# Kernel tuning notes

Hardware: AMD Instinct MI355X
Metric: run time of the kernel (lower is better)

The kernel has to match this reference:

```python
import jax, jax.numpy as jnp
import numpy as np

T, A, E, N, W, HID, FD = 4096, 1024, 512, 32768, 10, 150, 20
GI = 2 * A + E  # 2560
BINS = jnp.array([1, 2, 3, 4, 8, 16, 32, 64], dtype=jnp.int32)


def _mlp(x, W1, b1, W2, b2, W3, b3):
    # Score module: Linear->ReLU->Linear->ReLU->Linear->1 (dropout is a no-op in eval)
    h = jax.nn.relu(x @ W1 + b1)
    h = jax.nn.relu(h @ W2 + b2)
    return h @ W3 + b3


def setup_inputs() -> dict:
    key = jax.random.key(0)
    ks = jax.random.split(key, 20)
    s = 0.02
    inp = {
        "states": jax.random.normal(ks[0], (T, A), jnp.float32),
        "embeds": jax.random.normal(ks[1], (T, E), jnp.float32),
        "span_starts": jax.random.randint(ks[2], (N,), 0, T - W, jnp.int32),
        "span_widths": jax.random.randint(ks[3], (N,), 1, W + 1, jnp.int32),
        # attention Score params (input A)
        "Wa1": jax.random.normal(ks[4], (A, HID)) * s, "ba1": jnp.zeros((HID,)),
        "Wa2": jax.random.normal(ks[5], (HID, HID)) * s, "ba2": jnp.zeros((HID,)),
        "Wa3": jax.random.normal(ks[6], (HID, 1)) * s, "ba3": jnp.zeros((1,)),
        # width Feature embedding table: len(bins)+1 = 9 rows
        "width_emb": jax.random.normal(ks[7], (9, FD)) * s,
        # mention Score params (input GI + FD)
        "Ws1": jax.random.normal(ks[8], (GI + FD, HID)) * s, "bs1": jnp.zeros((HID,)),
        "Ws2": jax.random.normal(ks[9], (HID, HID)) * s, "bs2": jnp.zeros((HID,)),
        "Ws3": jax.random.normal(ks[10], (HID, 1)) * s, "bs3": jnp.zeros((1,)),
    }
    return inp


def reference(states, embeds, span_starts, span_widths,
              Wa1, ba1, Wa2, ba2, Wa3, ba3, width_emb,
              Ws1, bs1, Ws2, bs2, Ws3, bs3):
    # per-token attention logits  [T]
    attns = _mlp(states, Wa1, ba1, Wa2, ba2, Wa3, ba3).squeeze(-1)
    offs = jnp.arange(W)                                   # [W]
    pos = span_starts[:, None] + offs[None, :]             # [N, W]
    mask = offs[None, :] < span_widths[:, None]            # ragged span mask
    pos_c = jnp.clip(pos, 0, T - 1)
    logit = jnp.where(mask, attns[pos_c], -jnp.inf)        # [N, W]
    w = jax.nn.softmax(logit, axis=1)                      # per-span softmax
    attn_sum = jnp.einsum('nw,nwe->ne', w, embeds[pos_c])  # [N, E]
    ends = span_starts + span_widths - 1
    bin_idx = jnp.sum(span_widths[:, None] >= BINS[None, :], axis=1)
    size = width_emb[bin_idx]                              # [N, FD]
    g = jnp.concatenate([states[span_starts], states[ends], attn_sum, size], axis=1)
    scores = _mlp(g, Ws1, bs1, Ws2, bs2, Ws3, bs3).squeeze(-1)  # [N]
    return scores
```

## Files before the change

### kernel.cpp

```cpp
#include <hip/hip_runtime.h>
#include <math.h>

#define T_TOK 4096
#define A_DIM 1024
#define E_DIM 512
#define N_SPAN 32768
#define W_MAX 10
#define HID 150
#define FD 20

#define PR  160
#define KP2 160

#define WS_ATTNS 0
#define WS_PB    4096
#define WS_WPACK 1314816
#define WS_SB    1627856
#define WS_EB    3725008
#define PB_P0 0
#define PB_P1 655360
#define PB_P2 1310720
#define PB_P3 1966080
#define WP_ST  0
#define WP_V   491520
#define WP_A2  573440
#define WP_S2  599040
#define WP_WE1 624640
#define WP_TOTAL 626080
#define SB_PIECES 524288
#define EB_PIECES 262144
#define PK_ITEMS (WP_TOTAL + SB_PIECES + EB_PIECES)

typedef short  bf16x8 __attribute__((ext_vector_type(8)));
typedef float  f32x4  __attribute__((ext_vector_type(4)));

__device__ __forceinline__ float4 ld4(const float* p) { return *(const float4*)p; }

__device__ __forceinline__ unsigned short f2bf(float f) {
    unsigned u = __float_as_uint(f);
    unsigned r = u + 0x7fffu + ((u >> 16) & 1u);
    return (unsigned short)(r >> 16);
}
__device__ __forceinline__ float bf2f(short s) {
    return __uint_as_float(((unsigned)(unsigned short)s) << 16);
}
__device__ __forceinline__ bf16x8 cvt_frag(const float* p) {
    float4 u = ld4(p), v = ld4(p + 4);
    bf16x8 f;
    f[0] = (short)f2bf(u.x); f[1] = (short)f2bf(u.y);
    f[2] = (short)f2bf(u.z); f[3] = (short)f2bf(u.w);
    f[4] = (short)f2bf(v.x); f[5] = (short)f2bf(v.y);
    f[6] = (short)f2bf(v.z); f[7] = (short)f2bf(v.w);
    return f;
}

typedef const __attribute__((address_space(1))) unsigned int as1_u32;
typedef __attribute__((address_space(3))) unsigned int as3_u32;
__device__ __forceinline__ void dma16(const void* g, void* l) {
    __builtin_amdgcn_global_load_lds((as1_u32*)g, (as3_u32*)l, 16, 0, 0);
}
template<int N> __device__ __forceinline__ void waitv() {
    asm volatile("s_waitcnt vmcnt(%0)" :: "n"(N) : "memory");
}

__global__ __launch_bounds__(256) void prepack_kernel(
    const float* __restrict__ states, const float* __restrict__ embeds,
    const float* __restrict__ Wa1, const float* __restrict__ Ws1,
    const float* __restrict__ Wa2, const float* __restrict__ Ws2,
    const float* __restrict__ width_emb,
    unsigned short* __restrict__ wp, unsigned short* __restrict__ Sb,
    unsigned short* __restrict__ Eb)
{
    int idx = blockIdx.x * 256 + threadIdx.x;
    if (idx >= PK_ITEMS) return;
    if (idx < WP_TOTAL) {
        float v = 0.f;
        if (idx < WP_V) {
            int gidx = idx / 163840, r = idx % 163840;
            int ngrp = r / 81920, r2 = r % 81920;
            int c = r2 / 2560, d = r2 % 2560;
            int n = d >> 5, qsw = (d >> 3) & 3, off = d & 7;
            int q = qsw ^ ((n >> 1) & 3);
            int k = c * 32 + q * 8 + off;
            int gn = ngrp * 80 + n;
            const float* W = (gidx == 0) ? Wa1 : Ws1 + (size_t)(gidx - 1) * 1024 * HID;
            if (gn < HID) v = W[(size_t)k * HID + gn];
        } else if (idx < WP_A2) {
            int r = idx - WP_V;
            int ngrp = r / 40960, r2 = r % 40960;
            int c = r2 / 2560, d = r2 % 2560;
            int n = d >> 5, qsw = (d >> 3) & 3, off = d & 7;
            int q = qsw ^ ((n >> 1) & 3);
            int k = c * 32 + q * 8 + off;
            int gn = ngrp * 80 + n;
            if (gn < HID) v = Ws1[(size_t)(2048 + k) * HID + gn];
        } else if (idx < WP_S2) {
            int e = idx - WP_A2;
            int n = e / KP2, k = e % KP2;
            if (n < HID && k < HID) v = Wa2[(size_t)k * HID + n];
        } else if (idx < WP_WE1) {
            int e = idx - WP_S2;
            int n = e / KP2, k = e % KP2;
            if (n < HID && k < HID) v = Ws2[(size_t)k * HID + n];
        } else {
            int e = idx - WP_WE1;
            int b = e / KP2, n = e % KP2;
            if (n < HID)
                for (int k = 0; k < FD; ++k)
                    v = fmaf(width_emb[b * FD + k], Ws1[(size_t)(2560 + k) * HID + n], v);
        }
        wp[idx] = f2bf(v);
    } else if (idx < WP_TOTAL + SB_PIECES) {
        int p = idx - WP_TOTAL;
        int mb = p >> 11, r = p & 2047;
        int c = r >> 6, d8 = r & 63;
        int m = d8 >> 2, qsw = d8 & 3;
        int q = qsw ^ ((m >> 1) & 3);
        const float* src = states + (size_t)(mb * 16 + m) * A_DIM + c * 32 + q * 8;
        *(bf16x8*)(Sb + (size_t)p * 8) = cvt_frag(src);
    } else {
        int p = idx - WP_TOTAL - SB_PIECES;
        int mb = p >> 10, r = p & 1023;
        int c = r >> 6, d8 = r & 63;
        int m = d8 >> 2, qsw = d8 & 3;
        int q = qsw ^ ((m >> 1) & 3);
        const float* src = embeds + (size_t)(mb * 16 + m) * E_DIM + c * 32 + q * 8;
        *(bf16x8*)(Eb + (size_t)p * 8) = cvt_frag(src);
    }
}

template<int NC>
__device__ __forceinline__ void gemm_dma(
    const unsigned short* __restrict__ srcA, const unsigned short* __restrict__ srcB,
    unsigned short (*__restrict__ bufB)[2560], unsigned short (*__restrict__ bufA)[512],
    int lane, int l15, int quad, f32x4 (&acc)[5])
{
    const int swz = (quad ^ ((l15 >> 1) & 3)) * 8;
    const int bl = l15 * 32 + swz;
#define DMAC(c) { _Pragma("unroll")                                          \
        for (int i = 0; i < 5; ++i)                                          \
            dma16(srcB + (size_t)(c) * 2560 + i * 512 + lane * 8,            \
                  &bufB[(c) & 3][i * 512]);                                  \
        dma16(srcA + (size_t)(c) * 512 + lane * 8, &bufA[(c) & 3][0]); }
    DMAC(0);
    DMAC(1);
    DMAC(2);
#pragma unroll
    for (int c = 0; c < NC; ++c) {
        if (c + 3 < NC) DMAC(c + 3);
        if (c + 3 < NC)      waitv<18>();
        else if (c + 2 < NC) waitv<12>();
        else if (c + 1 < NC) waitv<6>();
        else                 waitv<0>();
        bf16x8 af = *(const bf16x8*)(&bufA[c & 3][0] + bl);
        const unsigned short* bb = &bufB[c & 3][0];
#pragma unroll
        for (int t = 0; t < 5; ++t) {
            bf16x8 bf = *(const bf16x8*)(bb + t * 512 + bl);
            acc[t] = __builtin_amdgcn_mfma_f32_16x16x32_bf16(af, bf, acc[t], 0, 0, 0);
        }
    }
#undef DMAC
}

__global__ __launch_bounds__(64) void token_kernel(
    const unsigned short* __restrict__ Sb, const unsigned short* __restrict__ Eb,
    const unsigned short* __restrict__ wp, unsigned short* __restrict__ Pb)
{
    __shared__ __align__(16) unsigned short bufB[4][2560];
    __shared__ __align__(16) unsigned short bufA[4][512];

    const int lane = threadIdx.x, l15 = lane & 15, quad = lane >> 4;
    const int task = blockIdx.x;

    f32x4 acc[5];
#pragma unroll
    for (int t = 0; t < 5; ++t)
#pragma unroll
        for (int i = 0; i < 4; ++i) acc[t][i] = 0.f;

    int m0, gidx, ngrp;
    if (task < 1536) {
        const int mb = task / 6;
        m0 = mb * 16;
        const int sub = task % 6;
        gidx = sub >> 1;
        ngrp = sub & 1;
        const unsigned short* srcA = Sb + (size_t)mb * 16384;
        const unsigned short* srcB = wp + WP_ST + gidx * 163840 + ngrp * 81920;
        gemm_dma<32>(srcA, srcB, bufB, bufA, lane, l15, quad, acc);
    } else {
        const int e = task - 1536;
        const int mb = e >> 1;
        m0 = mb * 16;
        ngrp = e & 1;
        gidx = 3;
        const unsigned short* srcA = Eb + (size_t)mb * 8192;
        const unsigned short* srcB = wp + WP_V + ngrp * 40960;
        gemm_dma<16>(srcA, srcB, bufB, bufA, lane, l15, quad, acc);
    }

    unsigned short* Pg = Pb + (size_t)gidx * 655360;
#pragma unroll
    for (int t = 0; t < 5; ++t) {
        const int col = ngrp * 80 + t * 16 + l15;
#pragma unroll
        for (int i = 0; i < 4; ++i)
            Pg[(size_t)(m0 + quad * 4 + i) * PR + col] =
                (col < HID) ? f2bf(acc[t][i]) : (unsigned short)0;
    }
}

__global__ __launch_bounds__(64) void attn_tail_kernel(
    const unsigned short* __restrict__ P0, const float* __restrict__ ba1,
    const unsigned short* __restrict__ wp, const float* __restrict__ ba2,
    const float* __restrict__ Wa3, const float* __restrict__ ba3,
    float* __restrict__ attns)
{
    const int t0 = blockIdx.x * 16;
    const int lane = threadIdx.x, l15 = lane & 15, quad = lane >> 4;

    f32x4 acc[10];
#pragma unroll
    for (int nt = 0; nt < 10; ++nt)
#pragma unroll
        for (int i = 0; i < 4; ++i) acc[nt][i] = 0.f;

    const unsigned short* prow = P0 + (size_t)(t0 + l15) * PR;
    const unsigned short* bb = wp + WP_A2 + l15 * KP2 + quad * 8;

#pragma unroll
    for (int c = 0; c < 5; ++c) {
        const int k0 = c * 32;
        const int kk = k0 + quad * 8;
        bf16x8 raw = *(const bf16x8*)(prow + kk);
        bf16x8 af;
#pragma unroll
        for (int j = 0; j < 8; ++j) {
            const float b = (kk + j < HID) ? ba1[kk + j] : 0.f;
            af[j] = (short)f2bf(fmaxf(bf2f(raw[j]) + b, 0.f));
        }
#pragma unroll
        for (int nt = 0; nt < 10; ++nt) {
            bf16x8 bf = *(const bf16x8*)(bb + nt * 16 * KP2 + k0);
            acc[nt] = __builtin_amdgcn_mfma_f32_16x16x32_bf16(af, bf, acc[nt], 0, 0, 0);
        }
    }

    float sc[4] = {0.f, 0.f, 0.f, 0.f};
#pragma unroll
    for (int nt = 0; nt < 10; ++nt) {
        const int col = nt * 16 + l15;
        const float w3 = (col < HID) ? Wa3[col] : 0.f;
        const float b2 = (col < HID) ? ba2[col] : 0.f;
#pragma unroll
        for (int i = 0; i < 4; ++i)
            sc[i] = fmaf(fmaxf(acc[nt][i] + b2, 0.f), w3, sc[i]);
    }
#pragma unroll
    for (int off = 8; off >= 1; off >>= 1)
#pragma unroll
        for (int i = 0; i < 4; ++i) sc[i] += __shfl_down(sc[i], off, 16);
    if (l15 == 0) {
        const float b3 = ba3[0];
#pragma unroll
        for (int i = 0; i < 4; ++i) attns[t0 + quad * 4 + i] = sc[i] + b3;
    }
}

__global__ __launch_bounds__(256) void span_kernel(
    const unsigned short* __restrict__ Pb, const float* __restrict__ attns,
    const unsigned short* __restrict__ wp,
    const int* __restrict__ span_starts, const int* __restrict__ span_widths,
    const float* __restrict__ bs1, const float* __restrict__ bs2,
    const float* __restrict__ Ws3, const float* __restrict__ bs3,
    float* __restrict__ out)
{
    __shared__ unsigned short sHb[32][168];
    __shared__ float s_wgt[32][W_MAX];
    __shared__ int s_st[32], s_wd[32], s_bin[32], s_oid[32], s_wdr[32];
    __shared__ float sPart[4][32];
    __shared__ float sb1[KP2];

    const int tid = threadIdx.x;
    const int n0s = blockIdx.x * 32;

    if (tid < KP2) sb1[tid] = (tid < HID) ? bs1[tid] : 0.f;
    int st = 0, wd = 0;
    if (tid < 32) {
        st = span_starts[n0s + tid];
        wd = span_widths[n0s + tid];
        s_wdr[tid] = wd;
    }
    __syncthreads();
    if (tid < 32) {
        int rank = 0;
#pragma unroll
        for (int j = 0; j < 32; ++j) {
            const int wj = s_wdr[j];
            rank += (wj < wd) || (wj == wd && j < tid);
        }
        s_st[rank] = st; s_wd[rank] = wd; s_oid[rank] = tid;
        s_bin[rank] = (wd >= 1) + (wd >= 2) + (wd >= 3) + (wd >= 4) +
                      (wd >= 8) + (wd >= 16) + (wd >= 32) + (wd >= 64);
        float lg[W_MAX];
        float m = -1e30f;
#pragma unroll
        for (int w = 0; w < W_MAX; ++w)
            if (w < wd) { float a = attns[st + w]; lg[w] = a; m = fmaxf(m, a); }
        float sum = 0.f;
#pragma unroll
        for (int w = 0; w < W_MAX; ++w) {
            float e = (w < wd) ? __expf(lg[w] - m) : 0.f;
            lg[w] = e; sum += e;
        }
        float inv = 1.f / sum;
#pragma unroll
        for (int w = 0; w < W_MAX; ++w) s_wgt[rank][w] = lg[w] * inv;
    }
    __syncthreads();

    {
        const unsigned short* P1b = Pb + PB_P1;
        const unsigned short* P2b = Pb + PB_P2;
        const unsigned short* P3b = Pb + PB_P3;
        const unsigned short* WEb = wp + WP_WE1;
        const int s = tid >> 3, jl = tid & 7;
        const int sst = s_st[s], swd = s_wd[s];
        const size_t rs = (size_t)sst * PR;
        const size_t re = (size_t)(sst + swd - 1) * PR;
        const size_t rb = (size_t)s_bin[s] * PR;
        for (int c = jl; c < 20; c += 8) {
            const int j = c * 8;
            bf16x8 u1 = *(const bf16x8*)(P1b + rs + j);
            bf16x8 u2 = *(const bf16x8*)(P2b + re + j);
            bf16x8 uw = *(const bf16x8*)(WEb + rb + j);
            float acc[8];
#pragma unroll
            for (int i = 0; i < 8; ++i)
                acc[i] = bf2f(u1[i]) + bf2f(u2[i]) + bf2f(uw[i]) + sb1[j + i];
#pragma unroll
            for (int w = 0; w < W_MAX; ++w) {
                if (w < swd) {
                    float wt = s_wgt[s][w];
                    bf16x8 uv = *(const bf16x8*)(P3b + rs + (size_t)w * PR + j);
#pragma unroll
                    for (int i = 0; i < 8; ++i)
                        acc[i] = fmaf(wt, bf2f(uv[i]), acc[i]);
                }
            }
            bf16x8 pk;
#pragma unroll
            for (int i = 0; i < 8; ++i) pk[i] = (short)f2bf(fmaxf(acc[i], 0.f));
            *(bf16x8*)&sHb[s][j] = pk;
        }
    }
    __syncthreads();

    const int wv = tid >> 6, lane = tid & 63, l15 = lane & 15, quad = lane >> 4;
    const int nb = (wv < 2) ? wv * 3 : 6 + (wv - 2) * 2;
    const int cnt = (wv < 2) ? 3 : 2;

    f32x4 a2[2][3];
#pragma unroll
    for (int mt = 0; mt < 2; ++mt)
#pragma unroll
        for (int t = 0; t < 3; ++t)
#pragma unroll
            for (int i = 0; i < 4; ++i) a2[mt][t][i] = 0.f;

#pragma unroll
    for (int c = 0; c < 5; ++c) {
        int k0 = c * 32;
        bf16x8 af0 = *(const bf16x8*)&sHb[l15][k0 + quad * 8];
        bf16x8 af1 = *(const bf16x8*)&sHb[16 + l15][k0 + quad * 8];
#pragma unroll
        for (int t = 0; t < 3; ++t) {
            if (t < cnt) {
                bf16x8 b = *(const bf16x8*)(wp + WP_S2 +
                            (size_t)((nb + t) * 16 + l15) * KP2 + k0 + quad * 8);
                a2[0][t] = __builtin_amdgcn_mfma_f32_16x16x32_bf16(af0, b, a2[0][t], 0, 0, 0);
                a2[1][t] = __builtin_amdgcn_mfma_f32_16x16x32_bf16(af1, b, a2[1][t], 0, 0, 0);
            }
        }
    }

    float sc[2][4];
#pragma unroll
    for (int mt = 0; mt < 2; ++mt)
#pragma unroll
        for (int i = 0; i < 4; ++i) sc[mt][i] = 0.f;
#pragma unroll
    for (int t = 0; t < 3; ++t) {
        if (t < cnt) {
            int col = (nb + t) * 16 + l15;
            float w3 = (col < HID) ? Ws3[col] : 0.f;
            float b2 = (col < HID) ? bs2[col] : 0.f;
#pragma unroll
            for (int mt = 0; mt < 2; ++mt)
#pragma unroll
                for (int i = 0; i < 4; ++i)
                    sc[mt][i] = fmaf(fmaxf(a2[mt][t][i] + b2, 0.f), w3, sc[mt][i]);
        }
    }
#pragma unroll
    for (int off = 8; off >= 1; off >>= 1)
#pragma unroll
        for (int mt = 0; mt < 2; ++mt)
#pragma unroll
            for (int i = 0; i < 4; ++i)
                sc[mt][i] += __shfl_down(sc[mt][i], off, 16);
    if (l15 == 0) {
#pragma unroll
        for (int mt = 0; mt < 2; ++mt)
#pragma unroll
            for (int i = 0; i < 4; ++i)
                sPart[wv][mt * 16 + quad * 4 + i] = sc[mt][i];
    }
    __syncthreads();
    if (tid < 32)
        out[n0s + s_oid[tid]] = sPart[0][tid] + sPart[1][tid] + sPart[2][tid] +
                                sPart[3][tid] + bs3[0];
}

extern "C" void kernel_launch(void* const* d_in, const int* in_sizes, int n_in,
                              void* d_out, int out_size, void* d_ws, size_t ws_size,
                              hipStream_t stream)
{
    const float* states      = (const float*)d_in[0];
    const float* embeds      = (const float*)d_in[1];
    const int*   span_starts = (const int*)d_in[2];
    const int*   span_widths = (const int*)d_in[3];
    const float* Wa1 = (const float*)d_in[4];
    const float* ba1 = (const float*)d_in[5];
    const float* Wa2 = (const float*)d_in[6];
    const float* ba2 = (const float*)d_in[7];
    const float* Wa3 = (const float*)d_in[8];
    const float* ba3 = (const float*)d_in[9];
    const float* width_emb = (const float*)d_in[10];
    const float* Ws1 = (const float*)d_in[11];
    const float* bs1 = (const float*)d_in[12];
    const float* Ws2 = (const float*)d_in[13];
    const float* bs2 = (const float*)d_in[14];
    const float* Ws3 = (const float*)d_in[15];
    const float* bs3 = (const float*)d_in[16];
    float* out = (float*)d_out;

    float* ws    = (float*)d_ws;
    float* attns = ws + WS_ATTNS;
    unsigned short* Pb    = (unsigned short*)(ws + WS_PB);
    unsigned short* wpack = (unsigned short*)(ws + WS_WPACK);
    unsigned short* Sb    = (unsigned short*)(ws + WS_SB);
    unsigned short* Eb    = (unsigned short*)(ws + WS_EB);

    hipLaunchKernelGGL(prepack_kernel, dim3((PK_ITEMS + 255) / 256), dim3(256), 0, stream,
                       states, embeds, Wa1, Ws1, Wa2, Ws2, width_emb,
                       wpack, Sb, Eb);
    hipLaunchKernelGGL(token_kernel, dim3(2048), dim3(64), 0, stream,
                       Sb, Eb, wpack, Pb);
    hipLaunchKernelGGL(attn_tail_kernel, dim3(T_TOK / 16), dim3(64), 0, stream,
                       Pb + PB_P0, ba1, wpack, ba2, Wa3, ba3, attns);
    hipLaunchKernelGGL(span_kernel, dim3(N_SPAN / 32), dim3(256), 0, stream,
                       Pb, attns, wpack, span_starts, span_widths,
                       bs1, bs2, Ws3, bs3, out);
}
```

Measured before the change: 149.0 us.

## Retile token GEMM to 64-row blocks with direct register double-buffering

Replaces the LDS-staged global_load_lds pipeline in the token projection GEMM with direct global-to-register loads that are double-buffered. Each wave now computes a 64x80 output tile (4 M-tiles by 5 N-tiles) rather than 16x80, so every B fragment is reused across four A tiles. The grid shrinks from 2048 to 512 blocks and is ordered so that neighbouring blocks share weight slices. The aim is to cut redundant weight traffic and LDS round trips, at the cost of many more accumulator registers and fewer waves to hide latency.

```diff
diff --git a/kernel.cpp b/kernel.cpp
--- a/kernel.cpp
+++ b/kernel.cpp
@@ -52,15 +52,6 @@
     f[4] = (short)f2bf(v.x); f[5] = (short)f2bf(v.y);
     f[6] = (short)f2bf(v.z); f[7] = (short)f2bf(v.w);
     return f;
-}
-
-typedef const __attribute__((address_space(1))) unsigned int as1_u32;
-typedef __attribute__((address_space(3))) unsigned int as3_u32;
-__device__ __forceinline__ void dma16(const void* g, void* l) {
-    __builtin_amdgcn_global_load_lds((as1_u32*)g, (as3_u32*)l, 16, 0, 0);
-}
-template<int N> __device__ __forceinline__ void waitv() {
-    asm volatile("s_waitcnt vmcnt(%0)" :: "n"(N) : "memory");
 }
 
 __global__ __launch_bounds__(256) void prepack_kernel(
@@ -129,86 +120,79 @@
     }
 }
 
-template<int NC>
-__device__ __forceinline__ void gemm_dma(
-    const unsigned short* __restrict__ srcA, const unsigned short* __restrict__ srcB,
-    unsigned short (*__restrict__ bufB)[2560], unsigned short (*__restrict__ bufA)[512],
-    int lane, int l15, int quad, f32x4 (&acc)[5])
-{
-    const int swz = (quad ^ ((l15 >> 1) & 3)) * 8;
-    const int bl = l15 * 32 + swz;
-#define DMAC(c) { _Pragma("unroll")                                          \
-        for (int i = 0; i < 5; ++i)                                          \
-            dma16(srcB + (size_t)(c) * 2560 + i * 512 + lane * 8,            \
-                  &bufB[(c) & 3][i * 512]);                                  \
-        dma16(srcA + (size_t)(c) * 512 + lane * 8, &bufA[(c) & 3][0]); }
-    DMAC(0);
-    DMAC(1);
-    DMAC(2);
+template<int NC, int ATILE>
+__device__ __forceinline__ void gemm_m64(
+    const unsigned short* __restrict__ pA,
+    const unsigned short* __restrict__ pB,
+    f32x4 (&acc)[4][5])
+{
+    bf16x8 a[2][4], bb[2][5];
+#define LDC(c, s) { _Pragma("unroll") \
+        for (int mt = 0; mt < 4; ++mt) \
+            a[s][mt] = *(const bf16x8*)(pA + (size_t)mt * ATILE + (size_t)(c) * 512); \
+        _Pragma("unroll") \
+        for (int t = 0; t < 5; ++t) \
+            bb[s][t] = *(const bf16x8*)(pB + (size_t)(c) * 2560 + t * 512); }
+    LDC(0, 0);
 #pragma unroll
     for (int c = 0; c < NC; ++c) {
-        if (c + 3 < NC) DMAC(c + 3);
-        if (c + 3 < NC)      waitv<18>();
-        else if (c + 2 < NC) waitv<12>();
-        else if (c + 1 < NC) waitv<6>();
-        else                 waitv<0>();
-        bf16x8 af = *(const bf16x8*)(&bufA[c & 3][0] + bl);
-        const unsigned short* bb = &bufB[c & 3][0];
-#pragma unroll
-        for (int t = 0; t < 5; ++t) {
-            bf16x8 bf = *(const bf16x8*)(bb + t * 512 + bl);
-            acc[t] = __builtin_amdgcn_mfma_f32_16x16x32_bf16(af, bf, acc[t], 0, 0, 0);
-        }
-    }
-#undef DMAC
+        const int s = c & 1;
+        if (c + 1 < NC) LDC(c + 1, s ^ 1);
+#pragma unroll
+        for (int mt = 0; mt < 4; ++mt)
+#pragma unroll
+            for (int t = 0; t < 5; ++t)
+                acc[mt][t] = __builtin_amdgcn_mfma_f32_16x16x32_bf16(
+                                 a[s][mt], bb[s][t], acc[mt][t], 0, 0, 0);
+    }
+#undef LDC
 }
 
 __global__ __launch_bounds__(64) void token_kernel(
     const unsigned short* __restrict__ Sb, const unsigned short* __restrict__ Eb,
     const unsigned short* __restrict__ wp, unsigned short* __restrict__ Pb)
 {
-    __shared__ __align__(16) unsigned short bufB[4][2560];
-    __shared__ __align__(16) unsigned short bufA[4][512];
-
     const int lane = threadIdx.x, l15 = lane & 15, quad = lane >> 4;
-    const int task = blockIdx.x;
-
-    f32x4 acc[5];
-#pragma unroll
-    for (int t = 0; t < 5; ++t)
-#pragma unroll
-        for (int i = 0; i < 4; ++i) acc[t][i] = 0.f;
-
-    int m0, gidx, ngrp;
-    if (task < 1536) {
-        const int mb = task / 6;
-        m0 = mb * 16;
-        const int sub = task % 6;
-        gidx = sub >> 1;
-        ngrp = sub & 1;
-        const unsigned short* srcA = Sb + (size_t)mb * 16384;
-        const unsigned short* srcB = wp + WP_ST + gidx * 163840 + ngrp * 81920;
-        gemm_dma<32>(srcA, srcB, bufB, bufA, lane, l15, quad, acc);
+    const int bl = l15 * 32 + ((quad ^ ((l15 >> 1) & 3)) * 8);
+    const int b = blockIdx.x;
+
+    f32x4 acc[4][5];
+#pragma unroll
+    for (int mt = 0; mt < 4; ++mt)
+#pragma unroll
+        for (int t = 0; t < 5; ++t)
+#pragma unroll
+            for (int i = 0; i < 4; ++i) acc[mt][t][i] = 0.f;
+
+    int mg, gidx, ngrp;
+    if (b < 384) {
+        const int x = b & 7, r = b >> 3;
+        const int s = r % 6, g = r / 6;
+        mg = g * 8 + x; gidx = s >> 1; ngrp = s & 1;
+        const unsigned short* pA = Sb + (size_t)mg * 4 * 16384 + bl;
+        const unsigned short* pB = wp + WP_ST + gidx * 163840 + ngrp * 81920 + bl;
+        gemm_m64<32, 16384>(pA, pB, acc);
     } else {
-        const int e = task - 1536;
-        const int mb = e >> 1;
-        m0 = mb * 16;
-        ngrp = e & 1;
-        gidx = 3;
-        const unsigned short* srcA = Eb + (size_t)mb * 8192;
-        const unsigned short* srcB = wp + WP_V + ngrp * 40960;
-        gemm_dma<16>(srcA, srcB, bufB, bufA, lane, l15, quad, acc);
+        const int e = b - 384;
+        const int x = e & 7, r = e >> 3;
+        const int s = r & 1, g = r >> 1;
+        mg = g * 8 + x; gidx = 3; ngrp = s;
+        const unsigned short* pA = Eb + (size_t)mg * 4 * 8192 + bl;
+        const unsigned short* pB = wp + WP_V + ngrp * 40960 + bl;
+        gemm_m64<16, 8192>(pA, pB, acc);
     }
 
     unsigned short* Pg = Pb + (size_t)gidx * 655360;
 #pragma unroll
-    for (int t = 0; t < 5; ++t) {
-        const int col = ngrp * 80 + t * 16 + l15;
-#pragma unroll
-        for (int i = 0; i < 4; ++i)
-            Pg[(size_t)(m0 + quad * 4 + i) * PR + col] =
-                (col < HID) ? f2bf(acc[t][i]) : (unsigned short)0;
-    }
+    for (int mt = 0; mt < 4; ++mt)
+#pragma unroll
+        for (int t = 0; t < 5; ++t) {
+            const int col = ngrp * 80 + t * 16 + l15;
+#pragma unroll
+            for (int i = 0; i < 4; ++i)
+                Pg[(size_t)(mg * 64 + mt * 16 + quad * 4 + i) * PR + col] =
+                    (col < HID) ? f2bf(acc[mt][t][i]) : (unsigned short)0;
+        }
 }
 
 __global__ __launch_bounds__(64) void attn_tail_kernel(
@@ -456,7 +440,7 @@
     hipLaunchKernelGGL(prepack_kernel, dim3((PK_ITEMS + 255) / 256), dim3(256), 0, stream,
                        states, embeds, Wa1, Ws1, Wa2, Ws2, width_emb,
                        wpack, Sb, Eb);
-    hipLaunchKernelGGL(token_kernel, dim3(2048), dim3(64), 0, stream,
+    hipLaunchKernelGGL(token_kernel, dim3(512), dim3(64), 0, stream,
                        Sb, Eb, wpack, Pb);
     hipLaunchKernelGGL(attn_tail_kernel, dim3(T_TOK / 16), dim3(64), 0, stream,
                        Pb + PB_P0, ba1, wpack, ba2, Wa3, ba3, attns);
```

Measured after the change: 158.4 us. 6.3% more time.
